# Kernel optimization log

Measured on AMD Instinct MI355X. Metric: run time of the kernel, lower is better.

## Reference

```python
import jax, jax.numpy as jnp
import numpy as np

B, FEW, NSN, NQ, NN = 256, 5, 5, 10, 512
M, D, H, L, NSYM = 200, 100, 450, 2, 70000
BETA, MARGIN = 5.0, 1.0


def _lstm_dir(x, W_ih, W_hh, b_ih, b_hh):
    # x: (T, B, in) -> outputs (T, B, H), final h (B, H). PyTorch gate order i,f,g,o.
    Bn, Hn = x.shape[1], W_hh.shape[1]
    def cell(carry, xt):
        h, c = carry
        g = xt @ W_ih.T + h @ W_hh.T + b_ih + b_hh
        i, f, gg, o = jnp.split(g, 4, axis=-1)
        c = jax.nn.sigmoid(f) * c + jax.nn.sigmoid(i) * jnp.tanh(gg)
        h = jax.nn.sigmoid(o) * jnp.tanh(c)
        return (h, c), h
    z = jnp.zeros((Bn, Hn), x.dtype)
    (hT, _), ys = jax.lax.scan(cell, (z, z), x)
    return ys, hT


def _bidir(x, Wih, Whh, bih, bhh):
    # Wih: (2, 4H, in) stacked [fwd, bwd]
    yf, hf = _lstm_dir(x, Wih[0], Whh[0], bih[0], bhh[0])
    yb, hb = _lstm_dir(x[::-1], Wih[1], Whh[1], bih[1], bhh[1])
    return jnp.concatenate([yf, yb[::-1]], -1), hf, hb


def setup_inputs():
    key = jax.random.key(0)
    ks = jax.random.split(key, 30)
    f32 = jnp.float32
    emb = jax.random.normal(ks[0], (NSYM + 1, D), f32) * 0.1
    emb = emb.at[NSYM].set(0.0)  # padding_idx
    s = 0.05
    inp = dict(
        support=jax.random.normal(ks[1], (B, FEW, 2, D), f32),
        support_negative=jax.random.normal(ks[2], (B, NSN, 2, D), f32),
        query=jax.random.normal(ks[3], (B, NQ, 2, D), f32),
        negative=jax.random.normal(ks[4], (B, NN, 2, D), f32),
        norm_vector=jax.random.normal(ks[5], (B, 1, 1, D), f32),
        left_conn=jax.random.randint(ks[6], (FEW, B, M, 3), 0, NSYM, jnp.int32),
        right_conn=jax.random.randint(ks[7], (FEW, B, M, 3), 0, NSYM, jnp.int32),
        symbol_emb=emb,
        gcn_w=jax.random.normal(ks[8], (D, 2 * D), f32) * s,
        gcn_wb=jnp.zeros((D,), f32),
        gcn_b=jnp.zeros((D,), f32),
        attn_w=jax.random.normal(ks[9], (1, D), f32) * s,
        attn_wb=jnp.zeros((1,), f32),
        gate_w=jax.random.normal(ks[10], (1, D), f32) * s,
        gate_wb=jnp.zeros((1,), f32),
        gate_b=jnp.zeros((1,), f32),
        Wih0=jax.random.normal(ks[11], (2, 4 * H, 2 * D), f32) * s,
        Whh0=jax.random.normal(ks[12], (2, 4 * H, H), f32) * s,
        bih0=jnp.zeros((2, 4 * H), f32),
        bhh0=jnp.zeros((2, 4 * H), f32),
        Wih1=jax.random.normal(ks[13], (2, 4 * H, 2 * H), f32) * s,
        Whh1=jax.random.normal(ks[14], (2, 4 * H, H), f32) * s,
        bih1=jnp.zeros((2, 4 * H), f32),
        bhh1=jnp.zeros((2, 4 * H), f32),
        out_w=jax.random.normal(ks[15], (D, 2 * H * L), f32) * s,
        out_b=jnp.zeros((D,), f32),
    )
    return inp


def reference(support, support_negative, query, negative, norm_vector,
              left_conn, right_conn, symbol_emb,
              gcn_w, gcn_wb, gcn_b, attn_w, attn_wb, gate_w, gate_wb, gate_b,
              Wih0, Whh0, bih0, bhh0, Wih1, Whh1, bih1, bhh1, out_w, out_b):
    few, b, m, _ = left_conn.shape
    d = symbol_emb.shape[1]

    def neighbor_encoder(conn):  # (N, M, 3) -> (N, D); dropout=identity (eval)
        rel_e = symbol_emb[conn[:, :, 1]]            # (N, M, D)
        ent_e = symbol_emb[conn[:, :, 2]]            # (N, M, D)
        self_e = symbol_emb[conn[:, 0, 0]]           # (N, D)
        cat = jnp.concatenate([rel_e, ent_e], -1)    # (N, M, 2D)
        out = jax.nn.leaky_relu(cat @ gcn_w.T + gcn_wb + gcn_b, 0.01)
        attn = jax.nn.softmax(out @ attn_w.T + attn_wb, axis=1)  # (N, M, 1)
        out_attn = jnp.einsum('nmd,nm->nd', out, attn[..., 0])
        gate = jax.nn.sigmoid(out_attn @ gate_w.T + gate_wb + gate_b)  # (N, 1)
        return out_attn * gate + self_e * (1.0 - gate)

    # all (few, left/right) encodings in one fused pass
    conn_all = jnp.stack([left_conn, right_conn], 1).reshape(few * 2 * b, m, 3)
    enc = neighbor_encoder(conn_all).reshape(few, 2, b, d).transpose(2, 0, 1, 3)  # (B, few, 2, D)

    # LSTM_attn relation learner
    x = enc.reshape(b, few, 2 * d).transpose(1, 0, 2)  # (T=few, B, 2D)
    y, h0f, h0b = _bidir(x, Wih0, Whh0, bih0, bhh0)
    y, h1f, h1b = _bidir(y, Wih1, Whh1, bih1, bhh1)
    final = jnp.stack([h0f, h0b, h1f, h1b], 0)         # (2*L, B, H)
    output = y.transpose(1, 0, 2)                       # (B, T, 2H)
    hidden = final.reshape(-1, 2 * H, L)                # faithful to torch .view
    aw = jax.nn.softmax(jnp.einsum('bth,bhl->btl', output, hidden), axis=1)
    context = jnp.einsum('bth,btl->bhl', output, aw).reshape(b, 2 * H * L)
    rel = (context @ out_w.T + out_b).reshape(b, 1, 1, d)

    def split_concat(pos, neg):
        e1 = jnp.concatenate([pos[:, :, 0, :], neg[:, :, 0, :]], 1)[:, :, None, :]
        e2 = jnp.concatenate([pos[:, :, 1, :], neg[:, :, 1, :]], 1)[:, :, None, :]
        return e1, e2

    def emb_learner(h, t, r, norm, pos_num):
        norm = norm[:, :1, :, :]
        h = h - jnp.sum(h * norm, -1, keepdims=True) * norm
        t = t - jnp.sum(t * norm, -1, keepdims=True) * norm
        score = -jnp.linalg.norm(h + r - t, axis=-1)[:, :, 0]
        return score[:, :pos_num], score[:, pos_num:]

    nsn = support_negative.shape[1]
    def inner_loss(rel_):
        rel_s = jnp.broadcast_to(rel_, (b, few + nsn, 1, d))
        e1, e2 = split_concat(support, support_negative)
        p, n = emb_learner(e1, e2, rel_s, norm_vector, few)
        return jnp.mean(jax.nn.relu(MARGIN - (p - n)))

    grad_meta = jax.grad(inner_loss)(rel)
    rel_q = rel - BETA * grad_meta
    norm_q = norm_vector - BETA * grad_meta

    nq, nn = query.shape[1], negative.shape[1]
    e1, e2 = split_concat(query, negative)
    rel_qe = jnp.broadcast_to(rel_q, (b, nq + nn, 1, d))
    p_score, n_score = emb_learner(e1, e2, rel_qe, norm_q, nq)
    return p_score, n_score
```

## Files before the change

### kernel.cpp

```cpp
#include <hip/hip_runtime.h>

typedef unsigned short u16;
typedef unsigned int   u32;
typedef __attribute__((ext_vector_type(8))) short short8;
typedef __attribute__((ext_vector_type(4))) float f32x4;

__device__ __forceinline__ float u2f(u32 u){
  union { u32 i; float f; } v; v.i = u << 16; return v.f;
}
__device__ __forceinline__ u16 f2bu(float f){
  union { float f; u32 i; } v; v.f = f;
  u32 i = v.i;
  i += 0x7fffu + ((i >> 16) & 1u);
  return (u16)(i >> 16);
}
__device__ __forceinline__ float sigm(float x){ return 1.0f/(1.0f + expf(-x)); }
__device__ __forceinline__ float ldf(const void* p, size_t i, int bf){
  return bf ? u2f(((const u16*)p)[i]) : ((const float*)p)[i];
}
__device__ __forceinline__ float wsum(float v){
  #pragma unroll
  for (int off = 32; off > 0; off >>= 1) v += __shfl_xor(v, off, 64);
  return v;
}

__global__ __launch_bounds__(64) void k_detect(const u32* __restrict__ nv,
                                               int* __restrict__ flag)
{
  int i = threadIdx.x;
  u32 w = nv[i];
  u32 e = (w >> 7) & 0xffu;
  bool sane = (e >= 100u && e <= 140u);
  unsigned long long m = __ballot(sane);
  if (i == 0) *flag = (__popcll(m) >= 40) ? 1 : 0;
}

__global__ __launch_bounds__(256) void k_pack(
    const void* __restrict__ src, u16* __restrict__ dst,
    int K, int Kp, int R, int Rp, const int* __restrict__ flag)
{
  const int bf = *flag;
  int total = Rp*Kp;
  int idx = blockIdx.x*256 + threadIdx.x;
  if (idx >= total) return;
  int r = idx / Kp, k = idx - r*Kp;
  u16 v = 0;
  if (k < K && r < R){
    size_t si = (size_t)r*K + k;
    v = bf ? ((const u16*)src)[si] : f2bu(((const float*)src)[si]);
  }
  dst[idx] = v;
}

__global__ __launch_bounds__(256) void k_packe(
    const void* __restrict__ emb, u16* __restrict__ Eb,
    int total4, const int* __restrict__ flag)
{
  const int bf = *flag;
  int idx = blockIdx.x*256 + threadIdx.x;
  if (idx >= total4) return;
  size_t i = (size_t)idx*4;
  union { u16 q[4]; uint2 d; } o;
  if (bf){
    o.d = *(const uint2*)((const u16*)emb + i);
  } else {
    float4 t = *(const float4*)((const float*)emb + i);
    o.q[0] = f2bu(t.x); o.q[1] = f2bu(t.y);
    o.q[2] = f2bu(t.z); o.q[3] = f2bu(t.w);
  }
  *(uint2*)(Eb + i) = o.d;
}

__global__ __launch_bounds__(256) void k_packg(
    const void* __restrict__ src, u16* __restrict__ dst,
    int K, int Kp, const int* __restrict__ flag)
{
  const int bf = *flag;
  const int Kq = Kp >> 2;
  const int per = 1920*Kq;
  int idx = blockIdx.x*256 + threadIdx.x;
  if (idx >= 2*per) return;
  int z = idx / per, r = idx - z*per;
  int rp = r / Kq, cq = r - rp*Kq;
  int c0 = cq*4;
  int kblk = rp >> 6, rem = rp & 63, gate = rem >> 4, klo = rem & 15;
  int k = kblk*16 + klo;
  union { u16 q[4]; uint2 d; } o;
  o.q[0] = 0; o.q[1] = 0; o.q[2] = 0; o.q[3] = 0;
  if (k < 450){
    size_t base = ((size_t)z*1800 + (size_t)gate*450 + k)*K;
    #pragma unroll
    for (int e = 0; e < 4; ++e){
      int c = c0 + e;
      if (c < K)
        o.q[e] = bf ? ((const u16*)src)[base+c] : f2bu(((const float*)src)[base+c]);
    }
  }
  *(uint2*)(dst + (size_t)idx*4) = o.d;
}

__global__ __launch_bounds__(256) void k_packb(
    const void* __restrict__ bih, const void* __restrict__ bhh,
    float* __restrict__ Bp, const int* __restrict__ flag)
{
  const int bf = *flag;
  int idx = blockIdx.x*256 + threadIdx.x;
  if (idx >= 2*1920) return;
  int z = idx / 1920, rp = idx - z*1920;
  int kblk = rp >> 6, rem = rp & 63, gate = rem >> 4, klo = rem & 15;
  int k = kblk*16 + klo;
  float v = 0.0f;
  if (k < 450){
    size_t si = (size_t)z*1800 + (size_t)gate*450 + k;
    v = ldf(bih, si, bf) + ldf(bhh, si, bf);
  }
  Bp[idx] = v;
}

__global__ __launch_bounds__(512, 4) void k_gcn(
    const int* __restrict__ left, const int* __restrict__ right,
    const void* __restrict__ emb, const u16* __restrict__ Eb,
    const u16* __restrict__ Wg,
    const void* __restrict__ gcnwb, const void* __restrict__ gcnb,
    const void* __restrict__ attnw, const void* __restrict__ attnwb,
    const void* __restrict__ gatew, const void* __restrict__ gatewb,
    const void* __restrict__ gateb,
    const int* __restrict__ flag,
    u16* __restrict__ X0bf)
{
  __shared__ __align__(16) u16 As[208*40];
  __shared__ __align__(16) u16 Bs[112*232];
  __shared__ int c1_s[200], c2_s[200];
  __shared__ float logit_s[208];
  __shared__ float red_s[512];
  __shared__ float attnw_s[112], bias_s[112], gatew_s[112], oa_s[112];

  const int bf  = *flag;
  const int tid = threadIdx.x;
  const int n   = blockIdx.x;
  const int b   = n & 255;
  const int fs  = n >> 8;
  const int s   = fs & 1;
  const int f   = fs >> 1;
  const int* conn = (s == 0 ? left : right) + (size_t)(f*256 + b)*600;

  if (tid < 200){ c1_s[tid] = conn[tid*3+1]; c2_s[tid] = conn[tid*3+2]; }
  if (tid < 112){
    attnw_s[tid] = (tid < 100) ? ldf(attnw, tid, bf) : 0.0f;
    bias_s[tid]  = (tid < 100) ? (ldf(gcnwb, tid, bf) + ldf(gcnb, tid, bf)) : 0.0f;
    gatew_s[tid] = (tid < 100) ? ldf(gatew, tid, bf) : 0.0f;
    oa_s[tid] = 0.0f;
  }
  for (int g = tid; g < 112*28; g += 512){
    int r = g / 28, cc = g - r*28;
    *(short8*)(Bs + r*232 + cc*8) = *(const short8*)(Wg + (size_t)r*224 + cc*8);
  }
  __syncthreads();

  const int wid  = tid >> 6, lane = tid & 63, ln = lane & 15, quad = lane >> 4;
  const int mt0 = (wid < 5) ? 2*wid : (10 + (wid - 5));
  const int nmt = (wid < 5) ? 2 : 1;

  auto loadA = [&](int kc, uint2* pv){
    #pragma unroll
    for (int it = 0; it < 4; ++it){
      int g = tid + it*512;
      uint2 v; v.x = 0u; v.y = 0u;
      if (g < 1664){
        int r = g >> 3, gi = g & 7, k = kc*32 + gi*4;
        if (r < 200 && k < 200){
          int c  = (k < 100) ? c1_s[r] : c2_s[r];
          int kk = (k < 100) ? k : (k - 100);
          v = *(const uint2*)(Eb + (size_t)c*100 + kk);
        }
      }
      pv[it] = v;
    }
  };

  f32x4 acc[2][7];
  #pragma unroll
  for (int i = 0; i < 2; ++i)
    #pragma unroll
    for (int j = 0; j < 7; ++j) acc[i][j] = (f32x4)0.0f;

  uint2 pv[4];
  loadA(0, pv);

  for (int kc = 0; kc < 7; ++kc){
    const int k0 = kc*32;
    #pragma unroll
    for (int it = 0; it < 4; ++it){
      int g = tid + it*512;
      if (g < 1664){
        int r = g >> 3, gi = g & 7;
        *(uint2*)(As + r*40 + gi*4) = pv[it];
      }
    }
    __syncthreads();
    if (kc < 6) loadA(kc+1, pv);

    #pragma unroll
    for (int mi = 0; mi < 2; ++mi){
      if (mi < nmt){
        short8 afr = *(const short8*)(As + ((mt0+mi)*16 + ln)*40 + quad*8);
        #pragma unroll
        for (int nt = 0; nt < 7; ++nt){
          short8 bfr = *(const short8*)(Bs + (size_t)(nt*16 + ln)*232 + k0 + quad*8);
          acc[mi][nt] = __builtin_amdgcn_mfma_f32_16x16x32_bf16(afr, bfr, acc[mi][nt], 0, 0, 0);
        }
      }
    }
    __syncthreads();
  }

  const float awb = ldf(attnwb, 0, bf);
  #pragma unroll
  for (int mi = 0; mi < 2; ++mi){
    if (mi < nmt){
      #pragma unroll
      for (int rg = 0; rg < 4; ++rg){
        float p = 0.0f;
        #pragma unroll
        for (int nt = 0; nt < 7; ++nt){
          float x = acc[mi][nt][rg] + bias_s[nt*16 + ln];
          x = x > 0.0f ? x : 0.01f*x;
          p += x * attnw_s[nt*16 + ln];
        }
        p += __shfl_xor(p, 1, 64); p += __shfl_xor(p, 2, 64);
        p += __shfl_xor(p, 4, 64); p += __shfl_xor(p, 8, 64);
        int m = (mt0+mi)*16 + quad*4 + rg;
        if (ln == 0 && m < 200) logit_s[m] = p + awb;
      }
    }
  }
  __syncthreads();

  red_s[tid] = (tid < 200) ? logit_s[tid] : -3.0e38f;
  __syncthreads();
  for (int off = 256; off > 0; off >>= 1){
    if (tid < off) red_s[tid] = fmaxf(red_s[tid], red_s[tid+off]);
    __syncthreads();
  }
  float mx = red_s[0];
  __syncthreads();
  float ev = 0.0f;
  if (tid < 200) ev = expf(logit_s[tid] - mx);
  red_s[tid] = ev;
  __syncthreads();
  for (int off = 256; off > 0; off >>= 1){
    if (tid < off) red_s[tid] += red_s[tid+off];
    __syncthreads();
  }
  float S = red_s[0];
  __syncthreads();
  if (tid < 208) logit_s[tid] = (tid < 200) ? ev*(1.0f/S) : 0.0f;
  __syncthreads();

  float at[2][4];
  #pragma unroll
  for (int mi = 0; mi < 2; ++mi)
    #pragma unroll
    for (int rg = 0; rg < 4; ++rg)
      at[mi][rg] = (mi < nmt) ? logit_s[(mt0+mi)*16 + quad*4 + rg] : 0.0f;

  #pragma unroll
  for (int nt = 0; nt < 7; ++nt){
    float p = 0.0f;
    #pragma unroll
    for (int mi = 0; mi < 2; ++mi){
      if (mi < nmt){
        #pragma unroll
        for (int rg = 0; rg < 4; ++rg){
          float x = acc[mi][nt][rg] + bias_s[nt*16 + ln];
          x = x > 0.0f ? x : 0.01f*x;
          p += x * at[mi][rg];
        }
      }
    }
    p += __shfl_xor(p, 16, 64); p += __shfl_xor(p, 32, 64);
    if (quad == 0) atomicAdd(&oa_s[nt*16 + ln], p);
  }
  __syncthreads();

  red_s[tid] = (tid < 100) ? oa_s[tid]*gatew_s[tid] : 0.0f;
  __syncthreads();
  for (int off = 256; off > 0; off >>= 1){
    if (tid < off) red_s[tid] += red_s[tid+off];
    __syncthreads();
  }
  float gate = sigm(red_s[0] + ldf(gatewb, 0, bf) + ldf(gateb, 0, bf));
  if (tid < 100){
    int c0 = conn[0];
    float self = ldf(emb, (size_t)c0*100 + tid, bf);
    X0bf[((size_t)f*256 + b)*224 + s*100 + tid] = f2bu(oa_s[tid]*gate + self*(1.0f - gate));
  }
}

__global__ __launch_bounds__(256) void k_mgemm(
    const u16* __restrict__ A, int lda, size_t Astride,
    const u16* __restrict__ B, int ldb, size_t Bstride,
    const float* __restrict__ bsum,
    u16* __restrict__ out, size_t Ostride,
    int N, int KC)
{
  __shared__ __align__(16) u16 As[128*40];
  __shared__ __align__(16) u16 Bs[128*40];
  const int tid = threadIdx.x;
  const int z  = blockIdx.z;
  const int nb = blockIdx.x, mb = blockIdx.y;
  const u16* Az = A + (size_t)z*Astride;
  const u16* Bz = B + (size_t)z*Bstride;

  const int wid = tid >> 6, lane = tid & 63, ln = lane & 15, quad = lane >> 4;
  const int wm = wid >> 1, wn = wid & 1;

  f32x4 acc[4][4];
  #pragma unroll
  for (int i = 0; i < 4; ++i)
    #pragma unroll
    for (int j = 0; j < 4; ++j) acc[i][j] = (f32x4)0.0f;

  const int srow = tid >> 1;
  const int koff = (tid & 1)*16;
  const int rowA = mb*128 + srow;
  const int rowB = nb*128 + srow;

  for (int kc = 0; kc < KC; ++kc){
    const int k0 = kc*32 + koff;
    const u16* ap = Az + (size_t)rowA*lda + k0;
    const u16* bp = Bz + (size_t)rowB*ldb + k0;
    short8 av0 = *(const short8*)(ap);
    short8 av1 = *(const short8*)(ap + 8);
    short8 bv0 = *(const short8*)(bp);
    short8 bv1 = *(const short8*)(bp + 8);
    *(short8*)(As + srow*40 + koff)     = av0;
    *(short8*)(As + srow*40 + koff + 8) = av1;
    *(short8*)(Bs + srow*40 + koff)     = bv0;
    *(short8*)(Bs + srow*40 + koff + 8) = bv1;
    __syncthreads();
    short8 af[4], bfr[4];
    #pragma unroll
    for (int i = 0; i < 4; ++i)
      af[i] = *(const short8*)(As + (wm*64 + i*16 + ln)*40 + quad*8);
    #pragma unroll
    for (int j = 0; j < 4; ++j)
      bfr[j] = *(const short8*)(Bs + (wn*64 + j*16 + ln)*40 + quad*8);
    #pragma unroll
    for (int i = 0; i < 4; ++i)
      #pragma unroll
      for (int j = 0; j < 4; ++j)
        acc[i][j] = __builtin_amdgcn_mfma_f32_16x16x32_bf16(af[i], bfr[j], acc[i][j], 0, 0, 0);
    __syncthreads();
  }

  #pragma unroll
  for (int j = 0; j < 4; ++j){
    int col = nb*128 + wn*64 + j*16 + ln;
    float bias = bsum ? bsum[(size_t)z*1920 + col] : 0.0f;
    #pragma unroll
    for (int i = 0; i < 4; ++i){
      #pragma unroll
      for (int rg = 0; rg < 4; ++rg){
        int row = mb*128 + wm*64 + i*16 + quad*4 + rg;
        out[(size_t)z*Ostride + (size_t)row*N + col] = f2bu(acc[i][j][rg] + bias);
      }
    }
  }
}

__global__ __launch_bounds__(64) void k_hstep(
    const u16* __restrict__ Hin, const u16* __restrict__ Whp,
    const u16* __restrict__ Gb, float* __restrict__ HC,
    u16* __restrict__ Hout, u16* __restrict__ Ybf, float* __restrict__ Yf,
    float* __restrict__ HF, int s, int layer)
{
  const int lane = threadIdx.x;
  const int ln = lane & 15, quad = lane >> 4;
  const int kb = blockIdx.x;
  const int mb = blockIdx.y;
  const int z  = blockIdx.z;

  const u16* Az = Hin + ((size_t)z*256 + mb*16)*480;
  const u16* Bz = Whp + (size_t)z*1920*480 + (size_t)kb*64*480;

  f32x4 acc[4];
  #pragma unroll
  for (int j = 0; j < 4; ++j) acc[j] = (f32x4)0.0f;

  #pragma unroll
  for (int kc = 0; kc < 15; ++kc){
    const int k0 = kc*32 + quad*8;
    short8 afr = *(const short8*)(Az + (size_t)ln*480 + k0);
    #pragma unroll
    for (int j = 0; j < 4; ++j){
      short8 bfr = *(const short8*)(Bz + (size_t)(j*16 + ln)*480 + k0);
      acc[j] = __builtin_amdgcn_mfma_f32_16x16x32_bf16(afr, bfr, acc[j], 0, 0, 0);
    }
  }

  const int k = kb*16 + ln;
  const int t = z ? (4 - s) : s;
  if (k < 450){
    const u16* Gz = Gb + (size_t)z*2457600 + (size_t)t*256*1920;
    #pragma unroll
    for (int rg = 0; rg < 4; ++rg){
      int b = mb*16 + quad*4 + rg;
      const u16* grow = Gz + (size_t)b*1920 + kb*64 + ln;
      float gi = acc[0][rg] + u2f(grow[0]);
      float gf = acc[1][rg] + u2f(grow[16]);
      float gg = acc[2][rg] + u2f(grow[32]);
      float go = acc[3][rg] + u2f(grow[48]);
      float* cp = HC + ((size_t)(2+z)*256 + b)*450 + k;
      float c = sigm(gf)*(*cp) + sigm(gi)*tanhf(gg);
      float h = sigm(go)*tanhf(c);
      *cp = c;
      Hout[((size_t)z*256 + b)*480 + k] = f2bu(h);
      if (Ybf) Ybf[((size_t)t*256 + b)*928 + z*450 + k] = f2bu(h);
      else     Yf [((size_t)t*256 + b)*900 + z*450 + k] = h;
      HF[((size_t)(layer*2+z)*256 + b)*450 + k] = h;
    }
  }
}

__global__ __launch_bounds__(256) void k_attn(
    const float* __restrict__ Y1, const float* __restrict__ HF,
    float* __restrict__ CTX)
{
  __shared__ float red2[40];
  __shared__ float aw[10];
  int b = blockIdx.x, tid = threadIdx.x;
  int wid = tid >> 6, lane = tid & 63;
  for (int p = 0; p < 10; ++p){
    int t = p >> 1, l = p & 1;
    float a = 0.0f;
    for (int h = tid; h < 900; h += 256)
      a += Y1[((size_t)t*256 + b)*900 + h] * HF[(size_t)b*1800 + h*2 + l];
    a = wsum(a);
    if (lane == 0) red2[p*4 + wid] = a;
  }
  __syncthreads();
  if (tid < 2){
    int l = tid;
    float sc[5];
    float mxv = -3.0e38f;
    for (int t = 0; t < 5; ++t){
      int p = t*2 + l;
      sc[t] = red2[p*4] + red2[p*4+1] + red2[p*4+2] + red2[p*4+3];
      mxv = fmaxf(mxv, sc[t]);
    }
    float e[5], sum = 0.0f;
    for (int t = 0; t < 5; ++t){ e[t] = expf(sc[t]-mxv); sum += e[t]; }
    for (int t = 0; t < 5; ++t) aw[t*2+l] = e[t]/sum;
  }
  __syncthreads();
  for (int h = tid; h < 900; h += 256){
    float v0 = 0.0f, v1 = 0.0f;
    for (int t = 0; t < 5; ++t){
      float y = Y1[((size_t)t*256 + b)*900 + h];
      v0 += y*aw[t*2+0]; v1 += y*aw[t*2+1];
    }
    CTX[(size_t)b*1800 + h*2 + 0] = v0;
    CTX[(size_t)b*1800 + h*2 + 1] = v1;
  }
}

__global__ __launch_bounds__(256) void k_gemm(
    const float* __restrict__ A, const void* __restrict__ W, size_t wEl,
    const void* __restrict__ b1, const void* __restrict__ b2, size_t bEl,
    const int* __restrict__ flag,
    float* __restrict__ out, int K, int C)
{
  extern __shared__ float a_s[];
  const int bf = *flag;
  const int tid = threadIdx.x;
  const int r = blockIdx.y;
  const float* a = A + (size_t)r*K;
  for (int k = tid; k < K; k += 256) a_s[k] = a[k];
  __syncthreads();
  const int j = blockIdx.x*256 + tid;
  if (j >= C) return;
  float acc = 0.0f;
  if (b1) acc += ldf(b1, bEl + j, bf);
  if (b2) acc += ldf(b2, bEl + j, bf);
  if (bf){
    const u16* w = (const u16*)W + wEl + (size_t)j*K;
    for (int k = 0; k < K; k += 4){
      uint2 wv = *(const uint2*)(w + k);
      acc += a_s[k]   * u2f(wv.x & 0xffffu);
      acc += a_s[k+1] * u2f(wv.x >> 16);
      acc += a_s[k+2] * u2f(wv.y & 0xffffu);
      acc += a_s[k+3] * u2f(wv.y >> 16);
    }
  } else {
    const float* w = (const float*)W + wEl + (size_t)j*K;
    for (int k = 0; k < K; k += 4){
      float4 wv = *(const float4*)(w + k);
      acc += a_s[k]*wv.x + a_s[k+1]*wv.y + a_s[k+2]*wv.z + a_s[k+3]*wv.w;
    }
  }
  out[(size_t)r*C + j] = acc;
}

__global__ __launch_bounds__(64) void k_grad(
    const void* __restrict__ sup, const void* __restrict__ supn,
    const void* __restrict__ normv, const float* __restrict__ REL,
    const int* __restrict__ flag,
    float* __restrict__ RELQ, float* __restrict__ NORMQ)
{
  const int bf = *flag;
  const int b = blockIdx.x, lane = threadIdx.x;
  const int d0 = lane, d1 = lane + 64;
  const bool a1 = (d1 < 100);
  float nv0 = ldf(normv, (size_t)b*100 + d0, bf);
  float nv1 = a1 ? ldf(normv, (size_t)b*100 + d1, bf) : 0.0f;
  float rl0 = REL[(size_t)b*100 + d0];
  float rl1 = a1 ? REL[(size_t)b*100 + d1] : 0.0f;
  float acc0 = 0.0f, acc1 = 0.0f;
  for (int j = 0; j < 5; ++j){
    size_t base = (size_t)(b*5+j)*200;
    float h10 = ldf(sup,  base + d0, bf);
    float t10 = ldf(sup,  base + 100 + d0, bf);
    float h20 = ldf(supn, base + d0, bf);
    float t20 = ldf(supn, base + 100 + d0, bf);
    float h11 = a1 ? ldf(sup,  base + d1, bf) : 0.0f;
    float t11 = a1 ? ldf(sup,  base + 100 + d1, bf) : 0.0f;
    float h21 = a1 ? ldf(supn, base + d1, bf) : 0.0f;
    float t21 = a1 ? ldf(supn, base + 100 + d1, bf) : 0.0f;
    float hd1 = wsum(h10*nv0 + h11*nv1);
    float td1 = wsum(t10*nv0 + t11*nv1);
    float hd2 = wsum(h20*nv0 + h21*nv1);
    float td2 = wsum(t20*nv0 + t21*nv1);
    float upd0 = (h10 - hd1*nv0) + rl0 - (t10 - td1*nv0);
    float upd1 = (h11 - hd1*nv1) + rl1 - (t11 - td1*nv1);
    float und0 = (h20 - hd2*nv0) + rl0 - (t20 - td2*nv0);
    float und1 = (h21 - hd2*nv1) + rl1 - (t21 - td2*nv1);
    if (!a1){ upd1 = 0.0f; und1 = 0.0f; }
    float np2 = wsum(upd0*upd0 + upd1*upd1);
    float nn2 = wsum(und0*und0 + und1*und1);
    float p = -sqrtf(np2), nsc = -sqrtf(nn2);
    if (1.0f - (p - nsc) > 0.0f){
      float ip = 1.0f/sqrtf(np2), in = 1.0f/sqrtf(nn2);
      acc0 += upd0*ip - und0*in;
      acc1 += upd1*ip - und1*in;
    }
  }
  float g0 = acc0 * (1.0f/1280.0f);
  RELQ [(size_t)b*100 + d0] = rl0 - 5.0f*g0;
  NORMQ[(size_t)b*100 + d0] = nv0 - 5.0f*g0;
  if (a1){
    float g1 = acc1 * (1.0f/1280.0f);
    RELQ [(size_t)b*100 + d1] = rl1 - 5.0f*g1;
    NORMQ[(size_t)b*100 + d1] = nv1 - 5.0f*g1;
  }
}

__global__ __launch_bounds__(256) void k_score(
    const void* __restrict__ query, const void* __restrict__ neg,
    const float* __restrict__ RELQ, const float* __restrict__ NORMQ,
    const int* __restrict__ flag, void* __restrict__ out)
{
  __shared__ __align__(16) float nq[104], rq[104];
  const int bf = *flag;
  const int b = blockIdx.x, tid = threadIdx.x;
  if (tid < 100){ nq[tid] = NORMQ[b*100+tid]; rq[tid] = RELQ[b*100+tid]; }
  __syncthreads();
  const int wid = tid >> 6, lane = tid & 63;
  const bool lo = (lane < 25);
  const bool hi = (lane >= 32 && lane < 57);
  const int d0 = lo ? lane*4 : (hi ? (lane-32)*4 : 0);
  float4 w4 = make_float4(0.0f,0.0f,0.0f,0.0f);
  float4 r4 = make_float4(0.0f,0.0f,0.0f,0.0f);
  if (lo || hi) w4 = *(const float4*)(nq + d0);
  if (lo)       r4 = *(const float4*)(rq + d0);

  for (int qi = blockIdx.y*4 + wid; qi < 522; qi += 32){
    const void* src = (qi < 10) ? query : neg;
    size_t row = (qi < 10) ? ((size_t)b*10 + qi) : ((size_t)b*512 + qi - 10);
    size_t base = row*200 + (hi ? 100 : 0) + d0;
    float4 v = make_float4(0.0f,0.0f,0.0f,0.0f);
    if (lo || hi){
      if (bf){
        uint2 u = *(const uint2*)((const u16*)src + base);
        v.x = u2f(u.x & 0xffffu); v.y = u2f(u.x >> 16);
        v.z = u2f(u.y & 0xffffu); v.w = u2f(u.y >> 16);
      } else {
        v = *(const float4*)((const float*)src + base);
      }
    }
    float pr = v.x*w4.x + v.y*w4.y + v.z*w4.z + v.w*w4.w;
    #pragma unroll
    for (int off = 16; off > 0; off >>= 1) pr += __shfl_xor(pr, off, 32);
    float tdv = __shfl(pr, lane + 32, 64);
    float4 t4;
    t4.x = __shfl(v.x, lane + 32, 64);
    t4.y = __shfl(v.y, lane + 32, 64);
    t4.z = __shfl(v.z, lane + 32, 64);
    t4.w = __shfl(v.w, lane + 32, 64);
    float s2 = 0.0f;
    if (lo){
      float ux = (v.x - pr*w4.x) + r4.x - (t4.x - tdv*w4.x);
      float uy = (v.y - pr*w4.y) + r4.y - (t4.y - tdv*w4.y);
      float uz = (v.z - pr*w4.z) + r4.z - (t4.z - tdv*w4.z);
      float uw = (v.w - pr*w4.w) + r4.w - (t4.w - tdv*w4.w);
      s2 = ux*ux + uy*uy + uz*uz + uw*uw;
    }
    #pragma unroll
    for (int off = 16; off > 0; off >>= 1) s2 += __shfl_xor(s2, off, 32);
    if (lane == 0){
      float sc = -sqrtf(s2);
      size_t oi = (qi < 10) ? ((size_t)b*10 + qi) : (2560 + (size_t)b*512 + (qi - 10));
      if (bf) ((u16*)out)[oi] = f2bu(sc);
      else    ((float*)out)[oi] = sc;
    }
  }
}

extern "C" void kernel_launch(void* const* d_in, const int* in_sizes, int n_in,
                              void* d_out, int out_size, void* d_ws, size_t ws_size,
                              hipStream_t stream)
{
  const void* support = d_in[0];
  const void* supneg  = d_in[1];
  const void* query   = d_in[2];
  const void* negat   = d_in[3];
  const void* normv   = d_in[4];
  const int* left     = (const int*)d_in[5];
  const int* right    = (const int*)d_in[6];
  const void* emb     = d_in[7];
  const void* gcnw    = d_in[8];
  const void* gcnwb   = d_in[9];
  const void* gcnb    = d_in[10];
  const void* attnw   = d_in[11];
  const void* attnwb  = d_in[12];
  const void* gatew   = d_in[13];
  const void* gatewb  = d_in[14];
  const void* gateb   = d_in[15];
  const void* Wih0    = d_in[16];
  const void* Whh0    = d_in[17];
  const void* bih0    = d_in[18];
  const void* bhh0    = d_in[19];
  const void* Wih1    = d_in[20];
  const void* Whh1    = d_in[21];
  const void* bih1    = d_in[22];
  const void* bhh1    = d_in[23];
  const void* outw    = d_in[24];
  const void* outb    = d_in[25];

  int*   dflag = (int*)d_ws;
  float* fws   = (float*)d_ws + 16;
  float* Y1   = fws;
  float* HF   = Y1 + 1152000;
  float* HC   = HF + 460800;
  float* CTX  = HC + 460800;
  float* RELb = CTX + 460800;
  float* RELQ = RELb + 25600;
  float* NORMQ= RELQ + 25600;
  float* Bp   = NORMQ + 25600;
  float* fend = Bp + 3840;
  u16* Gb   = (u16*)fend;
  u16* X0bf = Gb + 4915200;
  u16* Y0bf = X0bf + 286720;
  u16* Hbf  = Y0bf + 1187840;
  u16* Wg   = Hbf + 491520;
  u16* Eb   = Wg + 25088;
  u16* Wp   = Eb;
  u16* Whp  = Eb + 3563520;

  k_detect<<<1, 64, 0, stream>>>((const u32*)normv, dflag);

  hipMemsetAsync(X0bf, 0, 286720*sizeof(u16), stream);
  k_pack<<<(112*224+255)/256, 256, 0, stream>>>(gcnw, Wg, 200, 224, 100, 112, dflag);
  k_packe<<<(1750025+255)/256, 256, 0, stream>>>(emb, Eb, 1750025, dflag);
  k_gcn<<<2560, 512, 0, stream>>>(left, right, emb, Eb, Wg, gcnwb, gcnb,
                                  attnw, attnwb, gatew, gatewb, gateb,
                                  dflag, X0bf);

  u16* Hpar0 = Hbf;
  u16* Hpar1 = Hbf + 245760;

  hipMemsetAsync(Y0bf, 0, 1187840*sizeof(u16), stream);
  hipMemsetAsync(Hbf, 0, 491520*sizeof(u16), stream);
  hipMemsetAsync(HC, 0, 460800*sizeof(float), stream);
  k_packg<<<(2*1920*224/4+255)/256, 256, 0, stream>>>(Wih0, Wp, 200, 224, dflag);
  k_packg<<<(2*1920*480/4+255)/256, 256, 0, stream>>>(Whh0, Whp, 450, 480, dflag);
  k_packb<<<15, 256, 0, stream>>>(bih0, bhh0, Bp, dflag);
  k_mgemm<<<dim3(15,10,2), 256, 0, stream>>>(
      X0bf, 224, 0, Wp, 224, (size_t)1920*224,
      Bp, Gb, 2457600, 1920, 7);
  {
    u16* hc = Hpar0; u16* hn = Hpar1;
    for (int s = 0; s < 5; ++s){
      k_hstep<<<dim3(30,16,2), 64, 0, stream>>>(hc, Whp, Gb, HC, hn,
                                                Y0bf, nullptr, HF, s, 0);
      u16* tmp = hc; hc = hn; hn = tmp;
    }
  }

  hipMemsetAsync(Hbf, 0, 491520*sizeof(u16), stream);
  hipMemsetAsync(HC, 0, 460800*sizeof(float), stream);
  k_packg<<<(2*1920*928/4+255)/256, 256, 0, stream>>>(Wih1, Wp, 900, 928, dflag);
  k_packg<<<(2*1920*480/4+255)/256, 256, 0, stream>>>(Whh1, Whp, 450, 480, dflag);
  k_packb<<<15, 256, 0, stream>>>(bih1, bhh1, Bp, dflag);
  k_mgemm<<<dim3(15,10,2), 256, 0, stream>>>(
      Y0bf, 928, 0, Wp, 928, (size_t)1920*928,
      Bp, Gb, 2457600, 1920, 29);
  {
    u16* hc = Hpar0; u16* hn = Hpar1;
    for (int s = 0; s < 5; ++s){
      k_hstep<<<dim3(30,16,2), 64, 0, stream>>>(hc, Whp, Gb, HC, hn,
                                                nullptr, Y1, HF, s, 1);
      u16* tmp = hc; hc = hn; hn = tmp;
    }
  }

  k_attn<<<256, 256, 0, stream>>>(Y1, HF, CTX);
  k_gemm<<<dim3(1,256), 256, 1800*4, stream>>>(CTX, outw, 0, outb, nullptr, 0,
                                               dflag, RELb, 1800, 100);
  k_grad<<<256, 64, 0, stream>>>(support, supneg, normv, RELb, dflag, RELQ, NORMQ);
  k_score<<<dim3(256,8), 256, 0, stream>>>(query, negat, RELQ, NORMQ, dflag, d_out);
}
```

Measured before the change: 684.6 us.

## Fuse pack kernels and replace memsets with in-kernel zeroing and first-step skip

Merges the gcn-weight and embedding pack kernels into one launch, and merges the per-layer Wih/Whh/bias pack kernels into one launch. Removes the hipMemsetAsync calls for X0bf, Y0bf, Hbf and HC. Padding and state are now zeroed inside k_gcn and k_hstep, and the first time step skips the recurrent MFMA and the c-state read. This cuts launch count and memset traffic, at the risk of leaving padding regions unzeroed if the in-kernel zeroing misses any element the old memsets covered.

```diff
diff --git a/kernel.cpp b/kernel.cpp
--- a/kernel.cpp
+++ b/kernel.cpp
@@ -35,31 +35,26 @@
   if (i == 0) *flag = (__popcll(m) >= 40) ? 1 : 0;
 }
 
-__global__ __launch_bounds__(256) void k_pack(
-    const void* __restrict__ src, u16* __restrict__ dst,
-    int K, int Kp, int R, int Rp, const int* __restrict__ flag)
-{
-  const int bf = *flag;
-  int total = Rp*Kp;
-  int idx = blockIdx.x*256 + threadIdx.x;
-  if (idx >= total) return;
-  int r = idx / Kp, k = idx - r*Kp;
-  u16 v = 0;
-  if (k < K && r < R){
-    size_t si = (size_t)r*K + k;
-    v = bf ? ((const u16*)src)[si] : f2bu(((const float*)src)[si]);
-  }
-  dst[idx] = v;
-}
-
-__global__ __launch_bounds__(256) void k_packe(
+__global__ __launch_bounds__(256) void k_prep(
+    const void* __restrict__ gcnw, u16* __restrict__ Wg,
     const void* __restrict__ emb, u16* __restrict__ Eb,
-    int total4, const int* __restrict__ flag)
+    const int* __restrict__ flag)
 {
   const int bf = *flag;
   int idx = blockIdx.x*256 + threadIdx.x;
-  if (idx >= total4) return;
-  size_t i = (size_t)idx*4;
+  if (idx < 25088){
+    int r = idx / 224, k = idx - r*224;
+    u16 v = 0;
+    if (k < 200 && r < 100){
+      size_t si = (size_t)r*200 + k;
+      v = bf ? ((const u16*)gcnw)[si] : f2bu(((const float*)gcnw)[si]);
+    }
+    Wg[idx] = v;
+    return;
+  }
+  int e4 = idx - 25088;
+  if (e4 >= 1750025) return;
+  size_t i = (size_t)e4*4;
   union { u16 q[4]; uint2 d; } o;
   if (bf){
     o.d = *(const uint2*)((const u16*)emb + i);
@@ -71,15 +66,12 @@
   *(uint2*)(Eb + i) = o.d;
 }
 
-__global__ __launch_bounds__(256) void k_packg(
+__device__ __forceinline__ void packg_one(
     const void* __restrict__ src, u16* __restrict__ dst,
-    int K, int Kp, const int* __restrict__ flag)
-{
-  const int bf = *flag;
+    int K, int Kp, int bf, int idx)
+{
   const int Kq = Kp >> 2;
   const int per = 1920*Kq;
-  int idx = blockIdx.x*256 + threadIdx.x;
-  if (idx >= 2*per) return;
   int z = idx / per, r = idx - z*per;
   int rp = r / Kq, cq = r - rp*Kq;
   int c0 = cq*4;
@@ -99,12 +91,20 @@
   *(uint2*)(dst + (size_t)idx*4) = o.d;
 }
 
-__global__ __launch_bounds__(256) void k_packb(
+__global__ __launch_bounds__(256) void k_packL(
+    const void* __restrict__ Wih, int Kih, int KpIh, u16* __restrict__ Wp,
+    const void* __restrict__ Whh, u16* __restrict__ Whp,
     const void* __restrict__ bih, const void* __restrict__ bhh,
     float* __restrict__ Bp, const int* __restrict__ flag)
 {
   const int bf = *flag;
+  const int n1 = 2*1920*(KpIh >> 2);
+  const int n2 = 2*1920*120;
   int idx = blockIdx.x*256 + threadIdx.x;
+  if (idx < n1){ packg_one(Wih, Wp, Kih, KpIh, bf, idx); return; }
+  idx -= n1;
+  if (idx < n2){ packg_one(Whh, Whp, 450, 480, bf, idx); return; }
+  idx -= n2;
   if (idx >= 2*1920) return;
   int z = idx / 1920, rp = idx - z*1920;
   int kblk = rp >> 6, rem = rp & 63, gate = rem >> 4, klo = rem & 15;
@@ -155,6 +155,8 @@
     int r = g / 28, cc = g - r*28;
     *(short8*)(Bs + r*232 + cc*8) = *(const short8*)(Wg + (size_t)r*224 + cc*8);
   }
+  if (s == 1 && tid >= 100 && tid < 124)
+    X0bf[((size_t)f*256 + b)*224 + 100 + tid] = 0;
   __syncthreads();
 
   const int wid  = tid >> 6, lane = tid & 63, ln = lane & 15, quad = lane >> 4;
@@ -373,7 +375,7 @@
     const u16* __restrict__ Hin, const u16* __restrict__ Whp,
     const u16* __restrict__ Gb, float* __restrict__ HC,
     u16* __restrict__ Hout, u16* __restrict__ Ybf, float* __restrict__ Yf,
-    float* __restrict__ HF, int s, int layer)
+    float* __restrict__ HF, int s, int layer, int first)
 {
   const int lane = threadIdx.x;
   const int ln = lane & 15, quad = lane >> 4;
@@ -381,21 +383,22 @@
   const int mb = blockIdx.y;
   const int z  = blockIdx.z;
 
-  const u16* Az = Hin + ((size_t)z*256 + mb*16)*480;
-  const u16* Bz = Whp + (size_t)z*1920*480 + (size_t)kb*64*480;
-
   f32x4 acc[4];
   #pragma unroll
   for (int j = 0; j < 4; ++j) acc[j] = (f32x4)0.0f;
 
-  #pragma unroll
-  for (int kc = 0; kc < 15; ++kc){
-    const int k0 = kc*32 + quad*8;
-    short8 afr = *(const short8*)(Az + (size_t)ln*480 + k0);
-    #pragma unroll
-    for (int j = 0; j < 4; ++j){
-      short8 bfr = *(const short8*)(Bz + (size_t)(j*16 + ln)*480 + k0);
-      acc[j] = __builtin_amdgcn_mfma_f32_16x16x32_bf16(afr, bfr, acc[j], 0, 0, 0);
+  if (!first){
+    const u16* Az = Hin + ((size_t)z*256 + mb*16)*480;
+    const u16* Bz = Whp + (size_t)z*1920*480 + (size_t)kb*64*480;
+    #pragma unroll
+    for (int kc = 0; kc < 15; ++kc){
+      const int k0 = kc*32 + quad*8;
+      short8 afr = *(const short8*)(Az + (size_t)ln*480 + k0);
+      #pragma unroll
+      for (int j = 0; j < 4; ++j){
+        short8 bfr = *(const short8*)(Bz + (size_t)(j*16 + ln)*480 + k0);
+        acc[j] = __builtin_amdgcn_mfma_f32_16x16x32_bf16(afr, bfr, acc[j], 0, 0, 0);
+      }
     }
   }
 
@@ -412,13 +415,22 @@
       float gg = acc[2][rg] + u2f(grow[32]);
       float go = acc[3][rg] + u2f(grow[48]);
       float* cp = HC + ((size_t)(2+z)*256 + b)*450 + k;
-      float c = sigm(gf)*(*cp) + sigm(gi)*tanhf(gg);
+      float cprv = first ? 0.0f : *cp;
+      float c = sigm(gf)*cprv + sigm(gi)*tanhf(gg);
       float h = sigm(go)*tanhf(c);
       *cp = c;
       Hout[((size_t)z*256 + b)*480 + k] = f2bu(h);
       if (Ybf) Ybf[((size_t)t*256 + b)*928 + z*450 + k] = f2bu(h);
       else     Yf [((size_t)t*256 + b)*900 + z*450 + k] = h;
       HF[((size_t)(layer*2+z)*256 + b)*450 + k] = h;
+    }
+  } else {
+    #pragma unroll
+    for (int rg = 0; rg < 4; ++rg){
+      int b = mb*16 + quad*4 + rg;
+      Hout[((size_t)z*256 + b)*480 + k] = 0;
+      if (z == 1 && Ybf && k < 478)
+        Ybf[((size_t)t*256 + b)*928 + 450 + k] = 0;
     }
   }
 }
@@ -669,9 +681,7 @@
 
   k_detect<<<1, 64, 0, stream>>>((const u32*)normv, dflag);
 
-  hipMemsetAsync(X0bf, 0, 286720*sizeof(u16), stream);
-  k_pack<<<(112*224+255)/256, 256, 0, stream>>>(gcnw, Wg, 200, 224, 100, 112, dflag);
-  k_packe<<<(1750025+255)/256, 256, 0, stream>>>(emb, Eb, 1750025, dflag);
+  k_prep<<<(25088+1750025+255)/256, 256, 0, stream>>>(gcnw, Wg, emb, Eb, dflag);
   k_gcn<<<2560, 512, 0, stream>>>(left, right, emb, Eb, Wg, gcnwb, gcnb,
                                   attnw, attnwb, gatew, gatewb, gateb,
                                   dflag, X0bf);
@@ -679,12 +689,8 @@
   u16* Hpar0 = Hbf;
   u16* Hpar1 = Hbf + 245760;
 
-  hipMemsetAsync(Y0bf, 0, 1187840*sizeof(u16), stream);
-  hipMemsetAsync(Hbf, 0, 491520*sizeof(u16), stream);
-  hipMemsetAsync(HC, 0, 460800*sizeof(float), stream);
-  k_packg<<<(2*1920*224/4+255)/256, 256, 0, stream>>>(Wih0, Wp, 200, 224, dflag);
-  k_packg<<<(2*1920*480/4+255)/256, 256, 0, stream>>>(Whh0, Whp, 450, 480, dflag);
-  k_packb<<<15, 256, 0, stream>>>(bih0, bhh0, Bp, dflag);
+  k_packL<<<(2*1920*(224/4) + 2*1920*120 + 3840 + 255)/256, 256, 0, stream>>>(
+      Wih0, 200, 224, Wp, Whh0, Whp, bih0, bhh0, Bp, dflag);
   k_mgemm<<<dim3(15,10,2), 256, 0, stream>>>(
       X0bf, 224, 0, Wp, 224, (size_t)1920*224,
       Bp, Gb, 2457600, 1920, 7);
@@ -692,16 +698,13 @@
     u16* hc = Hpar0; u16* hn = Hpar1;
     for (int s = 0; s < 5; ++s){
       k_hstep<<<dim3(30,16,2), 64, 0, stream>>>(hc, Whp, Gb, HC, hn,
-                                                Y0bf, nullptr, HF, s, 0);
+                                                Y0bf, nullptr, HF, s, 0, s==0);
       u16* tmp = hc; hc = hn; hn = tmp;
     }
   }
 
-  hipMemsetAsync(Hbf, 0, 491520*sizeof(u16), stream);
-  hipMemsetAsync(HC, 0, 460800*sizeof(float), stream);
-  k_packg<<<(2*1920*928/4+255)/256, 256, 0, stream>>>(Wih1, Wp, 900, 928, dflag);
-  k_packg<<<(2*1920*480/4+255)/256, 256, 0, stream>>>(Whh1, Whp, 450, 480, dflag);
-  k_packb<<<15, 256, 0, stream>>>(bih1, bhh1, Bp, dflag);
+  k_packL<<<(2*1920*(928/4) + 2*1920*120 + 3840 + 255)/256, 256, 0, stream>>>(
+      Wih1, 900, 928, Wp, Whh1, Whp, bih1, bhh1, Bp, dflag);
   k_mgemm<<<dim3(15,10,2), 256, 0, stream>>>(
       Y0bf, 928, 0, Wp, 928, (size_t)1920*928,
       Bp, Gb, 2457600, 1920, 29);
@@ -709,7 +712,7 @@
     u16* hc = Hpar0; u16* hn = Hpar1;
     for (int s = 0; s < 5; ++s){
       k_hstep<<<dim3(30,16,2), 64, 0, stream>>>(hc, Whp, Gb, HC, hn,
-                                                nullptr, Y1, HF, s, 1);
+                                                nullptr, Y1, HF, s, 1, s==0);
       u16* tmp = hc; hc = hn; hn = tmp;
     }
   }
```

Result: faster. 644.0 us (-5.9%).
